# Performance work log

Measured on AMD Instinct MI355X. Metric: run time of the kernel, lower is better.

Reference implementation:

```python
import jax, jax.numpy as jnp
import numpy as np

B, C, H, W = 2, 128, 64, 64
D_STATE = 16
EXPAND = 2
D_INNER = C * EXPAND          # 256
DT_RANK = -(-C // 16)         # 8
K = 4                         # scan directions
COMPRESS = 3
SQUEEZE = 30
EPS = 1e-5


def layernorm(x, g, b):
    mu = x.mean(-1, keepdims=True)
    xm = x - mu
    var = (xm * xm).mean(-1, keepdims=True)
    return xm * jax.lax.rsqrt(var + EPS) * g + b


def conv2d(x, w, bias, pad):
    y = jax.lax.conv_general_dilated(x, w, (1, 1), ((pad, pad), (pad, pad)),
                                     dimension_numbers=('NCHW', 'OIHW', 'NCHW'))
    return y + bias[None, :, None, None]


def selective_scan(xs, dts, A, Bs, Cs):
    # xs,dts: (B,K,D,L); A: (K,D,N); Bs,Cs: (B,K,N,L)
    dt_t = jnp.moveaxis(dts, -1, 0)
    x_t = jnp.moveaxis(xs, -1, 0)
    B_t = jnp.moveaxis(Bs, -1, 0)
    C_t = jnp.moveaxis(Cs, -1, 0)
    h0 = jnp.zeros(xs.shape[:3] + (A.shape[-1],), xs.dtype)

    def step(h, inp):
        dt_l, x_l, b_l, c_l = inp          # (B,K,D),(B,K,D),(B,K,N),(B,K,N)
        dA = jnp.exp(dt_l[..., None] * A)  # (B,K,D,N)
        h = dA * h + (dt_l * x_l)[..., None] * b_l[:, :, None, :]
        y = jnp.einsum('bkdn,bkn->bkd', h, c_l)
        return h, y

    _, ys = jax.lax.scan(step, h0, (dt_t, x_t, B_t, C_t))
    return jnp.moveaxis(ys, 0, -1)  # (B,K,D,L)


def ss2d(x, p):  # x: (B,H,W,C) -> (B,H,W,C)
    xz = x @ p['in_proj_w'].T
    xc, z = jnp.split(xz, 2, axis=-1)
    xc = xc.transpose(0, 3, 1, 2)  # (B,D,H,W)
    xc = jax.lax.conv_general_dilated(xc, p['conv_w'], (1, 1), ((1, 1), (1, 1)),
                                      feature_group_count=D_INNER,
                                      dimension_numbers=('NCHW', 'OIHW', 'NCHW'))
    xc = jax.nn.silu(xc + p['conv_b'][None, :, None, None])
    b, d, h, w = xc.shape
    L = h * w
    x_hw = xc.reshape(b, d, L)
    x_wh = xc.transpose(0, 1, 3, 2).reshape(b, d, L)
    xs = jnp.stack([x_hw, x_wh, x_hw[..., ::-1], x_wh[..., ::-1]], axis=1)  # (B,4,D,L)
    x_dbl = jnp.einsum('bkdl,kcd->bkcl', xs, p['x_proj_w'])
    dtr, Bs, Cs = jnp.split(x_dbl, [DT_RANK, DT_RANK + D_STATE], axis=2)
    dts = jnp.einsum('bkrl,kdr->bkdl', dtr, p['dt_w'])
    dts = jax.nn.softplus(dts + p['dt_b'][None, :, :, None])
    A = -jnp.exp(p['A_logs']).reshape(K, d, D_STATE)
    ys = selective_scan(xs, dts, A, Bs, Cs)
    ys = ys + xs * p['Ds'].reshape(K, d)[None, :, :, None]
    inv = ys[:, 2:4][..., ::-1]  # undo flipped scans
    wh = lambda t: t.reshape(b, d, w, h).transpose(0, 1, 3, 2).reshape(b, d, L)
    y = ys[:, 0] + inv[:, 0] + wh(ys[:, 1]) + wh(inv[:, 1])
    y = y.transpose(0, 2, 1).reshape(b, h, w, d)
    y = layernorm(y, p['out_norm_g'], p['out_norm_b'])
    y = y * jax.nn.silu(z)
    return y @ p['out_proj_w'].T


def cab(x, p):  # x: (B,C,H,W)
    t = jax.nn.gelu(conv2d(x, p['cab_w1'], p['cab_b1'], 1), approximate=False)
    t = conv2d(t, p['cab_w2'], p['cab_b2'], 1)
    s = t.mean((2, 3), keepdims=True)
    s = jax.nn.relu(conv2d(s, p['ca_w1'], p['ca_b1'], 0))
    s = jax.nn.sigmoid(conv2d(s, p['ca_w2'], p['ca_b2'], 0))
    return t * s


def vss_block(input, p):
    inp = input.transpose(0, 2, 3, 1)  # (B,H,W,C)
    x = inp * p['skip_scale'] + ss2d(layernorm(inp, p['ln1_g'], p['ln1_b']), p)
    c = cab(layernorm(x, p['ln2_g'], p['ln2_b']).transpose(0, 3, 1, 2), p)
    x = x * p['skip_scale2'] + c.transpose(0, 2, 3, 1)
    return x.transpose(0, 3, 1, 2)


def setup_inputs() -> dict:
    key = jax.random.key(0)
    ks = jax.random.split(key, 16)
    rn = lambda i, shp, s=0.02: jax.random.normal(ks[i], shp, jnp.float32) * s
    return {
        'input': jax.random.normal(ks[0], (B, C, H, W), jnp.float32),
        'ln1_g': jnp.ones((C,), jnp.float32), 'ln1_b': jnp.zeros((C,), jnp.float32),
        'skip_scale': jnp.ones((C,), jnp.float32), 'skip_scale2': jnp.ones((C,), jnp.float32),
        'ln2_g': jnp.ones((C,), jnp.float32), 'ln2_b': jnp.zeros((C,), jnp.float32),
        'in_proj_w': rn(1, (2 * D_INNER, C)),
        'conv_w': rn(2, (D_INNER, 1, 3, 3), 0.1),
        'conv_b': jnp.zeros((D_INNER,), jnp.float32),
        'x_proj_w': rn(3, (K, DT_RANK + 2 * D_STATE, D_INNER)),
        'dt_w': rn(4, (K, D_INNER, DT_RANK), 0.1),
        'dt_b': rn(5, (K, D_INNER), 0.1),
        'A_logs': jnp.log(jnp.tile(jnp.arange(1, D_STATE + 1, dtype=jnp.float32), (K * D_INNER, 1))),
        'Ds': jnp.ones((K * D_INNER,), jnp.float32),
        'out_norm_g': jnp.ones((D_INNER,), jnp.float32), 'out_norm_b': jnp.zeros((D_INNER,), jnp.float32),
        'out_proj_w': rn(6, (C, D_INNER)),
        'cab_w1': rn(7, (C // COMPRESS, C, 3, 3), 0.05),
        'cab_b1': jnp.zeros((C // COMPRESS,), jnp.float32),
        'cab_w2': rn(8, (C, C // COMPRESS, 3, 3), 0.05),
        'cab_b2': jnp.zeros((C,), jnp.float32),
        'ca_w1': rn(9, (C // SQUEEZE, C, 1, 1), 0.05),
        'ca_b1': jnp.zeros((C // SQUEEZE,), jnp.float32),
        'ca_w2': rn(10, (C, C // SQUEEZE, 1, 1), 0.05),
        'ca_b2': jnp.zeros((C,), jnp.float32),
    }


def reference(input, ln1_g, ln1_b, skip_scale, skip_scale2, ln2_g, ln2_b,
              in_proj_w, conv_w, conv_b, x_proj_w, dt_w, dt_b, A_logs, Ds,
              out_norm_g, out_norm_b, out_proj_w,
              cab_w1, cab_b1, cab_w2, cab_b2, ca_w1, ca_b1, ca_w2, ca_b2):
    p = dict(ln1_g=ln1_g, ln1_b=ln1_b, skip_scale=skip_scale, skip_scale2=skip_scale2,
             ln2_g=ln2_g, ln2_b=ln2_b, in_proj_w=in_proj_w, conv_w=conv_w, conv_b=conv_b,
             x_proj_w=x_proj_w, dt_w=dt_w, dt_b=dt_b, A_logs=A_logs, Ds=Ds,
             out_norm_g=out_norm_g, out_norm_b=out_norm_b, out_proj_w=out_proj_w,
             cab_w1=cab_w1, cab_b1=cab_b1, cab_w2=cab_w2, cab_b2=cab_b2,
             ca_w1=ca_w1, ca_b1=ca_b1, ca_w2=ca_w2, ca_b2=ca_b2)
    return vss_block(input, p)
```

## Files before the change

### kernel.cpp

```cpp
#include <hip/hip_runtime.h>
#include <math.h>

#define BB 2
#define CC 128
#define HH 64
#define WW 64
#define LL 4096
#define DI 256
#define NS 16
#define KK 4
#define OC1 42

#define NC 256
#define CL 16

#define K3_POS 16
#define BCW 48

__device__ __forceinline__ float sigmoidf_(float x) { return 1.f / (1.f + __expf(-x)); }
__device__ __forceinline__ float siluf_(float x)    { return x * sigmoidf_(x); }

__device__ __forceinline__ int scan_pos(int k, int i) {
  if (k == 0) return i;
  if (k == 1) return ((i & 63) << 6) | (i >> 6);
  if (k == 2) return (LL - 1) - i;
  int j = (LL - 1) - i;
  return ((j & 63) << 6) | (j >> 6);
}

__global__ __launch_bounds__(256) void k1_ln_inproj(
    const float* __restrict__ inp, const float* __restrict__ g, const float* __restrict__ b,
    const float* __restrict__ wproj, float* __restrict__ xcin, float* __restrict__ zbuf) {
  __shared__ float sx[64][132];
  __shared__ float sw[128][68];
  __shared__ float smu[64], srs[64];
  const int tid = threadIdx.x;
  const int rt = blockIdx.x & 3;
  const int pt = blockIdx.x >> 2;
  const int bb = pt >> 6;
  const int pbase = (pt & 63) << 6;

  for (int idx = tid; idx < 64 * CC; idx += 256) {
    int c = idx >> 6, pl = idx & 63;
    sx[pl][c] = inp[((size_t)bb * CC + c) * LL + pbase + pl];
  }
  __syncthreads();
  {
    int pl = tid >> 2, j = tid & 3;
    float s = 0.f, s2 = 0.f;
    for (int c = j; c < CC; c += 4) { float v = sx[pl][c]; s += v; s2 += v * v; }
    s += __shfl_xor(s, 1); s2 += __shfl_xor(s2, 1);
    s += __shfl_xor(s, 2); s2 += __shfl_xor(s2, 2);
    if (j == 0) {
      float mu = s * (1.f / CC);
      smu[pl] = mu;
      srs[pl] = rsqrtf(s2 * (1.f / CC) - mu * mu + 1e-5f);
    }
  }
  __syncthreads();
  for (int idx = tid; idx < 64 * CC; idx += 256) {
    int c = idx & 127, pl = idx >> 7;
    sx[pl][c] = (sx[pl][c] - smu[pl]) * srs[pl] * g[c] + b[c];
  }

  const int pg = tid & 7, rg = tid >> 3;
  float acc[8][4];
#pragma unroll
  for (int j = 0; j < 8; j++)
#pragma unroll
    for (int q = 0; q < 4; q++) acc[j][q] = 0.f;

  for (int kc = 0; kc < CC; kc += 64) {
    __syncthreads();
    for (int idx = tid; idx < 128 * 64; idx += 256) {
      int cl = idx & 63, rl = idx >> 6;
      sw[rl][cl] = wproj[(size_t)(rt * 128 + rl) * CC + kc + cl];
    }
    __syncthreads();
#pragma unroll 4
    for (int i = 0; i < 16; i++) {
      const int k0 = kc + 4 * i, kl0 = 4 * i;
      float4 xv[8], wv[4];
#pragma unroll
      for (int j = 0; j < 8; j++) xv[j] = *(const float4*)&sx[pg + 8 * j][k0];
#pragma unroll
      for (int q = 0; q < 4; q++) wv[q] = *(const float4*)&sw[rg + 32 * q][kl0];
#pragma unroll
      for (int j = 0; j < 8; j++)
#pragma unroll
        for (int q = 0; q < 4; q++) {
          acc[j][q] += xv[j].x * wv[q].x + xv[j].y * wv[q].y
                     + xv[j].z * wv[q].z + xv[j].w * wv[q].w;
        }
    }
  }

  float* buf = (rt < 2) ? xcin : zbuf;
  const int drow = (rt & 1) * 128;
#pragma unroll
  for (int j = 0; j < 8; j++) {
    const int p = pbase + pg + 8 * j;
    float* dst = buf + ((size_t)bb * LL + p) * DI + drow;
#pragma unroll
    for (int q = 0; q < 4; q++) dst[rg + 32 * q] = acc[j][q];
  }
}

__global__ __launch_bounds__(256) void k2_dwconv(
    const float* __restrict__ xcin, const float* __restrict__ cw, const float* __restrict__ cb,
    float* __restrict__ xconv) {
  const int w0 = (blockIdx.x & 7) * 8;
  const int hh = (blockIdx.x >> 3) & 63;
  const int bb = blockIdx.x >> 9;
  const int d = threadIdx.x;

  float wv[9];
#pragma unroll
  for (int kk = 0; kk < 9; kk++) wv[kk] = cw[d * 9 + kk];
  const float bias = cb[d];

  float xin[3][10];
#pragma unroll
  for (int kh = 0; kh < 3; kh++) {
    int r = hh + kh - 1;
    bool vr = (r >= 0 && r < HH);
#pragma unroll
    for (int c = 0; c < 10; c++) {
      int cc2 = w0 + c - 1;
      bool vc = (cc2 >= 0 && cc2 < WW);
      xin[kh][c] = (vr && vc) ? xcin[((size_t)bb * LL + r * WW + cc2) * DI + d] : 0.f;
    }
  }
#pragma unroll
  for (int j = 0; j < 8; j++) {
    float acc = bias;
#pragma unroll
    for (int kh = 0; kh < 3; kh++)
#pragma unroll
      for (int kw = 0; kw < 3; kw++)
        acc += wv[kh * 3 + kw] * xin[kh][j + kw];
    xconv[((size_t)bb * LL + hh * WW + w0 + j) * DI + d] = siluf_(acc);
  }
}

__global__ __launch_bounds__(256) void k3_proj(
    const float* __restrict__ xconv, const float* __restrict__ xpw,
    float* __restrict__ BCbuf) {
  __shared__ float sv[K3_POS][260];
  const int tid = threadIdx.x;
  const int bb = blockIdx.x >> 8;
  const int pbase = (blockIdx.x & 255) << 4;

  for (int idx = tid; idx < K3_POS * DI; idx += 256) {
    int d = idx & 255, pl = idx >> 8;
    sv[pl][d] = xconv[((size_t)bb * LL + pbase + pl) * DI + d];
  }
  __syncthreads();

  const int rb = tid >> 4, pg = tid & 15;
  const int r0 = rb * 10;
  float acc[10];
#pragma unroll
  for (int q = 0; q < 10; q++) acc[q] = 0.f;

  const float4* wf = (const float4*)xpw;
#pragma unroll 4
  for (int i = 0; i < DI / 4; i++) {
    float4 xv = *(const float4*)&sv[pg][i * 4];
#pragma unroll
    for (int q = 0; q < 10; q++) {
      float4 wa = wf[(size_t)(r0 + q) * 64 + i];
      acc[q] += wa.x * xv.x + wa.y * xv.y + wa.z * xv.z + wa.w * xv.w;
    }
  }

  const int k = r0 / 40, c0 = r0 - k * 40;
  float* dst = BCbuf + ((size_t)(bb * KK + k) * LL + pbase + pg) * BCW + c0;
#pragma unroll
  for (int q = 0; q < 10; q++) dst[q] = acc[q];
}

__global__ __launch_bounds__(256) void k4a_chunk(
    const float* __restrict__ xconv, const float* __restrict__ BCbuf,
    const float* __restrict__ A_logs, const float* __restrict__ dtw,
    const float* __restrict__ dtb,
    float* __restrict__ csA, float* __restrict__ csB) {
  __shared__ float sBC[CL][26];
  const int d = threadIdx.x;
  const int chunk = blockIdx.x & (NC - 1);
  const int t = blockIdx.x / NC;
  const int k = t & 3;
  const int bb = t >> 2;
  const int bk = bb * KK + k;
  const int base = chunk * CL;

  for (int idx = d; idx < CL * 24; idx += 256) {
    int ii = idx / 24, j = idx - ii * 24;
    int pos = scan_pos(k, base + ii);
    sBC[ii][j] = BCbuf[((size_t)bk * LL + pos) * BCW + j];
  }
  float a[NS];
  bool fast = true;
#pragma unroll
  for (int n = 0; n < NS; n++) {
    a[n] = -__expf(A_logs[((size_t)k * DI + d) * NS + n]);
    fast = fast && (fabsf(a[n] + (float)(n + 1)) < 1e-3f * (n + 1));
  }
  const float* wdt = dtw + ((size_t)k * DI + d) * 8;
  const float4 wd0 = *(const float4*)wdt;
  const float4 wd1 = *(const float4*)(wdt + 4);
  const float bdt = dtb[k * DI + d];
  __syncthreads();

  const float* x_p = xconv + (size_t)bb * LL * DI + d;

  float Ap[NS], Bc[NS];
#pragma unroll
  for (int n = 0; n < NS; n++) { Ap[n] = 1.f; Bc[n] = 0.f; }

  if (fast) {
    float sumdt = 0.f;
#pragma unroll
    for (int half = 0; half < CL / 8; half++) {
      float xvr[8];
#pragma unroll
      for (int j = 0; j < 8; j++)
        xvr[j] = x_p[(size_t)scan_pos(k, base + half * 8 + j) * DI];
#pragma unroll
      for (int j = 0; j < 8; j++) {
        const int ii = half * 8 + j;
        const float* dr = sBC[ii];
        float u = bdt + wd0.x * dr[0] + wd0.y * dr[1] + wd0.z * dr[2] + wd0.w * dr[3]
                      + wd1.x * dr[4] + wd1.y * dr[5] + wd1.z * dr[6] + wd1.w * dr[7];
        float t2 = __expf(u);
        float E = __builtin_amdgcn_rcpf(1.f + t2);
        float dt = u > 20.f ? u : -0.69314718056f * __log2f(E);
        sumdt += dt;
        float dtx = dt * xvr[j];
        float E2 = E * E;
        float dA1 = E, dA2 = E2;
#pragma unroll
        for (int n = 0; n < NS; n += 2) {
          Bc[n] = dA1 * Bc[n] + dtx * sBC[ii][8 + n];
          Bc[n + 1] = dA2 * Bc[n + 1] + dtx * sBC[ii][9 + n];
          dA1 *= E2; dA2 *= E2;
        }
      }
    }
    float Et = __expf(-sumdt);
    float p = Et;
#pragma unroll
    for (int n = 0; n < NS; n++) { Ap[n] = p; p *= Et; }
  } else {
#pragma unroll 2
    for (int ii = 0; ii < CL; ii++) {
      int pos = scan_pos(k, base + ii);
      float xv = x_p[(size_t)pos * DI];
      const float* dr = sBC[ii];
      float u = bdt + wd0.x * dr[0] + wd0.y * dr[1] + wd0.z * dr[2] + wd0.w * dr[3]
                    + wd1.x * dr[4] + wd1.y * dr[5] + wd1.z * dr[6] + wd1.w * dr[7];
      float t2 = __expf(u);
      float dt = u > 20.f ? u : log1pf(t2);
      float dtx = dt * xv;
#pragma unroll
      for (int n = 0; n < NS; n++) {
        float dA = __expf(dt * a[n]);
        Ap[n] *= dA;
        Bc[n] = dA * Bc[n] + dtx * sBC[ii][8 + n];
      }
    }
  }
  size_t e = ((size_t)(bk * NC + chunk) * NS) * DI + d;
#pragma unroll
  for (int n = 0; n < NS; n++) {
    csA[e + (size_t)n * DI] = Ap[n];
    csB[e + (size_t)n * DI] = Bc[n];
  }
}

__global__ __launch_bounds__(256) void k4b_scanchunks(
    float* csAh, const float* __restrict__ csB) {
  const int d = threadIdx.x;
  const int n = blockIdx.x & (NS - 1);
  const int bk = blockIdx.x >> 4;
  const size_t stride = (size_t)NS * DI;
  size_t e = ((size_t)bk * NC * NS + n) * DI + d;
  float H = 0.f;
  for (int c0 = 0; c0 < NC; c0 += 16) {
    float A[16], Bv[16];
#pragma unroll
    for (int j = 0; j < 16; j++) {
      A[j]  = csAh[e + (size_t)j * stride];
      Bv[j] = csB[e + (size_t)j * stride];
    }
#pragma unroll
    for (int j = 0; j < 16; j++) {
      csAh[e + (size_t)j * stride] = H;
      H = A[j] * H + Bv[j];
    }
    e += (size_t)16 * stride;
  }
}

__global__ __launch_bounds__(256) void k4c_scan(
    const float* __restrict__ xconv, const float* __restrict__ BCbuf,
    const float* __restrict__ A_logs, const float* __restrict__ dtw,
    const float* __restrict__ dtb, const float* __restrict__ Ds,
    const float* __restrict__ hin, float* __restrict__ ys) {
  __shared__ float sBC[CL][BCW];
  const int d = threadIdx.x;
  const int chunk = blockIdx.x & (NC - 1);
  const int t = blockIdx.x / NC;
  const int k = t & 3;
  const int bb = t >> 2;
  const int bk = bb * KK + k;
  const int base = chunk * CL;

  for (int idx = d; idx < CL * 40; idx += 256) {
    int ii = idx / 40, j = idx - ii * 40;
    int pos = scan_pos(k, base + ii);
    sBC[ii][j] = BCbuf[((size_t)bk * LL + pos) * BCW + j];
  }
  float a[NS], h[NS];
  bool fast = true;
  const size_t eh = ((size_t)(bk * NC + chunk) * NS) * DI + d;
#pragma unroll
  for (int n = 0; n < NS; n++) {
    a[n] = -__expf(A_logs[((size_t)k * DI + d) * NS + n]);
    fast = fast && (fabsf(a[n] + (float)(n + 1)) < 1e-3f * (n + 1));
    h[n] = hin[eh + (size_t)n * DI];
  }
  const float* wdt = dtw + ((size_t)k * DI + d) * 8;
  const float4 wd0 = *(const float4*)wdt;
  const float4 wd1 = *(const float4*)(wdt + 4);
  const float bdt = dtb[k * DI + d];
  const float Dd = Ds[k * DI + d];
  __syncthreads();

  const float* x_p = xconv + (size_t)bb * LL * DI + d;
  float* ys_p = ys + (size_t)bk * LL * DI + d;

  if (fast) {
#pragma unroll
    for (int half = 0; half < CL / 8; half++) {
      float xvr[8];
#pragma unroll
      for (int j = 0; j < 8; j++)
        xvr[j] = x_p[(size_t)scan_pos(k, base + half * 8 + j) * DI];
#pragma unroll
      for (int j = 0; j < 8; j++) {
        const int ii = half * 8 + j;
        const float* dr = sBC[ii];
        float u = bdt + wd0.x * dr[0] + wd0.y * dr[1] + wd0.z * dr[2] + wd0.w * dr[3]
                      + wd1.x * dr[4] + wd1.y * dr[5] + wd1.z * dr[6] + wd1.w * dr[7];
        float t2 = __expf(u);
        float E = __builtin_amdgcn_rcpf(1.f + t2);
        float dt = u > 20.f ? u : -0.69314718056f * __log2f(E);
        float dtx = dt * xvr[j];
        float y = xvr[j] * Dd;
        float E2 = E * E;
        float dA1 = E, dA2 = E2;
#pragma unroll
        for (int n = 0; n < NS; n += 2) {
          h[n] = dA1 * h[n] + dtx * sBC[ii][8 + n];
          y += h[n] * sBC[ii][24 + n];
          h[n + 1] = dA2 * h[n + 1] + dtx * sBC[ii][9 + n];
          y += h[n + 1] * sBC[ii][25 + n];
          dA1 *= E2; dA2 *= E2;
        }
        ys_p[(size_t)scan_pos(k, base + ii) * DI] = y;
      }
    }
  } else {
#pragma unroll 2
    for (int ii = 0; ii < CL; ii++) {
      int pos = scan_pos(k, base + ii);
      float xv = x_p[(size_t)pos * DI];
      const float* dr = sBC[ii];
      float u = bdt + wd0.x * dr[0] + wd0.y * dr[1] + wd0.z * dr[2] + wd0.w * dr[3]
                    + wd1.x * dr[4] + wd1.y * dr[5] + wd1.z * dr[6] + wd1.w * dr[7];
      float t2 = __expf(u);
      float dt = u > 20.f ? u : log1pf(t2);
      float dtx = dt * xv;
      float y = xv * Dd;
#pragma unroll
      for (int n = 0; n < NS; n++) {
        float dA = __expf(dt * a[n]);
        h[n] = dA * h[n] + dtx * sBC[ii][8 + n];
        y += h[n] * sBC[ii][24 + n];
      }
      ys_p[(size_t)pos * DI] = y;
    }
  }
}

__global__ __launch_bounds__(256) void k5a_act(
    const float* __restrict__ ys, const float* __restrict__ zbuf,
    const float* __restrict__ ong, const float* __restrict__ onb,
    float* __restrict__ yact) {
  __shared__ float sy[8][260];
  __shared__ float smu[8], srs[8];
  const int tid = threadIdx.x;
  const int bb = blockIdx.x >> 9;
  const int pbase = (blockIdx.x & 511) << 3;

  for (int idx = tid; idx < 8 * DI; idx += 256) {
    int d = idx & 255, pl = idx >> 8;
    size_t o0 = (((size_t)bb * KK + 0) * LL + pbase + pl) * DI + d;
    const size_t st = (size_t)LL * DI;
    sy[pl][d] = ys[o0] + ys[o0 + st] + ys[o0 + 2 * st] + ys[o0 + 3 * st];
  }
  __syncthreads();
  {
    int pl = tid >> 5, j = tid & 31;
    float s = 0.f, s2 = 0.f;
    for (int d = j; d < DI; d += 32) { float v = sy[pl][d]; s += v; s2 += v * v; }
#pragma unroll
    for (int m = 1; m < 32; m <<= 1) { s += __shfl_xor(s, m); s2 += __shfl_xor(s2, m); }
    if (j == 0) {
      float mu = s * (1.f / DI);
      smu[pl] = mu;
      srs[pl] = rsqrtf(s2 * (1.f / DI) - mu * mu + 1e-5f);
    }
  }
  __syncthreads();
  for (int idx = tid; idx < 8 * DI; idx += 256) {
    int d = idx & 255, pl = idx >> 8;
    float zv = zbuf[((size_t)bb * LL + pbase + pl) * DI + d];
    yact[((size_t)bb * LL + pbase + pl) * DI + d] =
        ((sy[pl][d] - smu[pl]) * srs[pl] * ong[d] + onb[d]) * siluf_(zv);
  }
}

__global__ __launch_bounds__(256) void k5b_proj(
    const float* __restrict__ yact, const float* __restrict__ opw,
    const float* __restrict__ inp, const float* __restrict__ sk,
    const float* __restrict__ g2, const float* __restrict__ b2,
    float* __restrict__ xres, float* __restrict__ ln2) {
  __shared__ float sx[16][68];
  __shared__ float sw[128][68];
  __shared__ float sr[16][132];
  __shared__ float smu[16], srs[16];
  const int tid = threadIdx.x;
  const int bb = blockIdx.x >> 8;
  const int pbase = (blockIdx.x & 255) << 4;

  const int pg = tid & 7, rb = tid >> 3;
  float acc[2][4];
#pragma unroll
  for (int j = 0; j < 2; j++)
#pragma unroll
    for (int q = 0; q < 4; q++) acc[j][q] = 0.f;

  for (int kc = 0; kc < DI; kc += 64) {
    __syncthreads();
    for (int idx = tid; idx < 16 * 64; idx += 256) {
      int cl = idx & 63, pl = idx >> 6;
      sx[pl][cl] = yact[((size_t)bb * LL + pbase + pl) * DI + kc + cl];
    }
    for (int idx = tid; idx < 128 * 64; idx += 256) {
      int cl = idx & 63, rl = idx >> 6;
      sw[rl][cl] = opw[(size_t)rl * DI + kc + cl];
    }
    __syncthreads();
#pragma unroll 4
    for (int i = 0; i < 16; i++) {
      float4 xv[2], wv[4];
#pragma unroll
      for (int j = 0; j < 2; j++) xv[j] = *(const float4*)&sx[2 * pg + j][4 * i];
#pragma unroll
      for (int q = 0; q < 4; q++) wv[q] = *(const float4*)&sw[rb + 32 * q][4 * i];
#pragma unroll
      for (int j = 0; j < 2; j++)
#pragma unroll
        for (int q = 0; q < 4; q++) {
          acc[j][q] += xv[j].x * wv[q].x + xv[j].y * wv[q].y
                     + xv[j].z * wv[q].z + xv[j].w * wv[q].w;
        }
    }
  }

#pragma unroll
  for (int j = 0; j < 2; j++) {
    const int p = pbase + 2 * pg + j;
#pragma unroll
    for (int q = 0; q < 4; q++) {
      const int c = rb + 32 * q;
      float r = inp[((size_t)bb * CC + c) * LL + p] * sk[c] + acc[j][q];
      xres[((size_t)bb * LL + p) * CC + c] = r;
      sr[2 * pg + j][c] = r;
    }
  }
  __syncthreads();
  {
    int pl = tid >> 4, jj = tid & 15;
    float s = 0.f, s2 = 0.f;
    for (int c = jj; c < CC; c += 16) { float v = sr[pl][c]; s += v; s2 += v * v; }
#pragma unroll
    for (int m = 1; m < 16; m <<= 1) { s += __shfl_xor(s, m); s2 += __shfl_xor(s2, m); }
    if (jj == 0) {
      float mu = s * (1.f / CC);
      smu[pl] = mu;
      srs[pl] = rsqrtf(s2 * (1.f / CC) - mu * mu + 1e-5f);
    }
  }
  __syncthreads();
  for (int idx = tid; idx < 16 * CC; idx += 256) {
    int pl = idx & 15, c = idx >> 4;
    ln2[((size_t)bb * CC + c) * LL + pbase + pl] =
        (sr[pl][c] - smu[pl]) * srs[pl] * g2[c] + b2[c];
  }
}

__global__ __launch_bounds__(256) void k6a_conv1(
    const float* __restrict__ ln2, const float* __restrict__ w1,
    float* __restrict__ pc1) {
  __shared__ float sIn[16][6][68];
  __shared__ float sw[16 * 9 * OC1];
  const int tid = threadIdx.x;
  const int icq = blockIdx.x & 7;
  const int h4  = (blockIdx.x >> 3) & 15;
  const int bb  = blockIdx.x >> 7;
  const int icb = icq * 16;

  for (int idx = tid; idx < 16 * 6 * 66; idx += 256) {
    int i = idx / 396, rem = idx % 396;
    int rr = rem / 66, j = rem % 66;
    int r = h4 * 4 + rr - 1, c2 = j - 1;
    float v = 0.f;
    if (r >= 0 && r < HH && c2 >= 0 && c2 < WW)
      v = ln2[((size_t)bb * CC + icb + i) * LL + r * WW + c2];
    sIn[i][rr][j] = v;
  }
  for (int idx = tid; idx < OC1 * 16 * 9; idx += 256) {
    int oc = idx / 144, rem = idx % 144;
    int i = rem / 9, kk = rem % 9;
    sw[(i * 9 + kk) * OC1 + oc] = w1[((size_t)oc * CC + icb + i) * 9 + kk];
  }
  __syncthreads();

  const int wq = tid & 7, hq = (tid >> 3) & 3, ocg = tid >> 5;
  float acc[6][8];
#pragma unroll
  for (int q = 0; q < 6; q++)
#pragma unroll
    for (int ww = 0; ww < 8; ww++) acc[q][ww] = 0.f;

  for (int i = 0; i < 16; i++) {
    float xin[3][10];
#pragma unroll
    for (int kh = 0; kh < 3; kh++)
#pragma unroll
      for (int j = 0; j < 10; j++) xin[kh][j] = sIn[i][hq + kh][wq * 8 + j];
#pragma unroll
    for (int q = 0; q < 6; q++) {
      int oc = ocg + 8 * q;
      if (oc >= OC1) break;
      float wv[9];
#pragma unroll
      for (int kk = 0; kk < 9; kk++) wv[kk] = sw[(i * 9 + kk) * OC1 + oc];
#pragma unroll
      for (int kh = 0; kh < 3; kh++)
#pragma unroll
        for (int kw = 0; kw < 3; kw++)
#pragma unroll
          for (int ww = 0; ww < 8; ww++)
            acc[q][ww] += wv[kh * 3 + kw] * xin[kh][ww + kw];
    }
  }

  const int hrow = h4 * 4 + hq;
#pragma unroll
  for (int q = 0; q < 6; q++) {
    int oc = ocg + 8 * q;
    if (oc >= OC1) break;
    float* dst = pc1 + (((size_t)icq * BB + bb) * OC1 + oc) * LL + hrow * WW + wq * 8;
    *(float4*)dst       = make_float4(acc[q][0], acc[q][1], acc[q][2], acc[q][3]);
    *(float4*)(dst + 4) = make_float4(acc[q][4], acc[q][5], acc[q][6], acc[q][7]);
  }
}

__global__ __launch_bounds__(256) void k6b_reduce(
    const float* __restrict__ pc1, const float* __restrict__ b1,
    float* __restrict__ t1) {
  const int oc = blockIdx.x % OC1;
  const int bb = blockIdx.x / OC1;
  const float bias = b1[oc];
  const size_t st = (size_t)BB * OC1 * LL;
  const float* src = pc1 + ((size_t)bb * OC1 + oc) * LL;
  float* dst = t1 + ((size_t)bb * OC1 + oc) * LL;
  for (int i = threadIdx.x; i < LL / 4; i += 256) {
    float4 s = ((const float4*)src)[i];
#pragma unroll
    for (int icq = 1; icq < 8; icq++) {
      float4 v = *(const float4*)(src + (size_t)icq * st + i * 4);
      s.x += v.x; s.y += v.y; s.z += v.z; s.w += v.w;
    }
    float r[4] = {s.x + bias, s.y + bias, s.z + bias, s.w + bias};
#pragma unroll
    for (int q = 0; q < 4; q++)
      r[q] = 0.5f * r[q] * (1.f + erff(r[q] * 0.70710678118654752f));
    ((float4*)dst)[i] = make_float4(r[0], r[1], r[2], r[3]);
  }
}

__global__ __launch_bounds__(256) void k7_conv2(
    const float* __restrict__ t1, const float* __restrict__ w2, const float* __restrict__ b2,
    float* __restrict__ t2) {
  __shared__ float sIn[21][4][68];
  __shared__ float sw[21 * 9 * 32];
  const int tid = threadIdx.x;
  const int ocq = blockIdx.x & 3;
  const int h2  = (blockIdx.x >> 2) & 31;
  const int bb  = blockIdx.x >> 7;

  const int wq = tid & 7, hq = (tid >> 3) & 1, ocg = tid >> 4;
  float acc[2][8];
#pragma unroll
  for (int q = 0; q < 2; q++)
#pragma unroll
    for (int ww = 0; ww < 8; ww++) acc[q][ww] = 0.f;

  for (int ch = 0; ch < 2; ch++) {
    const int icb = ch * 21;
    __syncthreads();
    for (int idx = tid; idx < 21 * 4 * 66; idx += 256) {
      int i = idx / 264, rem = idx % 264;
      int rr = rem / 66, j = rem % 66;
      int r = h2 * 2 + rr - 1, c2 = j - 1;
      float v = 0.f;
      if (r >= 0 && r < HH && c2 >= 0 && c2 < WW)
        v = t1[((size_t)bb * OC1 + icb + i) * LL + r * WW + c2];
      sIn[i][rr][j] = v;
    }
    for (int idx = tid; idx < 32 * 21 * 9; idx += 256) {
      int ol = idx / 189, rem = idx % 189;
      int i = rem / 9, kk = rem % 9;
      sw[(i * 9 + kk) * 32 + ol] = w2[((size_t)(ocq * 32 + ol) * OC1 + icb + i) * 9 + kk];
    }
    __syncthreads();

    for (int i = 0; i < 21; i++) {
      float xin[3][10];
#pragma unroll
      for (int kh = 0; kh < 3; kh++)
#pragma unroll
        for (int j = 0; j < 10; j++) xin[kh][j] = sIn[i][hq + kh][wq * 8 + j];
#pragma unroll
      for (int q = 0; q < 2; q++) {
        int ol = ocg + 16 * q;
        float wv[9];
#pragma unroll
        for (int kk = 0; kk < 9; kk++) wv[kk] = sw[(i * 9 + kk) * 32 + ol];
#pragma unroll
        for (int kh = 0; kh < 3; kh++)
#pragma unroll
          for (int kw = 0; kw < 3; kw++)
#pragma unroll
            for (int ww = 0; ww < 8; ww++)
              acc[q][ww] += wv[kh * 3 + kw] * xin[kh][ww + kw];
      }
    }
  }

  const int hrow = h2 * 2 + hq;
#pragma unroll
  for (int q = 0; q < 2; q++) {
    int oc = ocq * 32 + ocg + 16 * q;
    float bias = b2[oc];
    float* dst = t2 + ((size_t)bb * CC + oc) * LL + hrow * WW + wq * 8;
    *(float4*)dst       = make_float4(acc[q][0] + bias, acc[q][1] + bias,
                                      acc[q][2] + bias, acc[q][3] + bias);
    *(float4*)(dst + 4) = make_float4(acc[q][4] + bias, acc[q][5] + bias,
                                      acc[q][6] + bias, acc[q][7] + bias);
  }
}

__global__ __launch_bounds__(256) void k8_mean(const float* __restrict__ t2,
                                               float* __restrict__ smean) {
  __shared__ float red[4];
  const int bc = blockIdx.x;
  const float* src = t2 + (size_t)bc * LL;
  float s = 0.f;
  for (int i = threadIdx.x; i < LL; i += 256) s += src[i];
#pragma unroll
  for (int m = 1; m < 64; m <<= 1) s += __shfl_xor(s, m);
  if ((threadIdx.x & 63) == 0) red[threadIdx.x >> 6] = s;
  __syncthreads();
  if (threadIdx.x == 0) smean[bc] = (red[0] + red[1] + red[2] + red[3]) * (1.f / LL);
}

__global__ __launch_bounds__(256) void k10_final(
    const float* __restrict__ xres, const float* __restrict__ t2,
    const float* __restrict__ smean,
    const float* __restrict__ cw1, const float* __restrict__ cb1,
    const float* __restrict__ cw2, const float* __restrict__ cb2,
    const float* __restrict__ sk2, float* __restrict__ out) {
  __shared__ float mid[4];
  const int tid = threadIdx.x;
  const int bc = blockIdx.x;
  const int bb = bc >> 7, c = bc & 127;

  {
    const int wv = tid >> 6, ln = tid & 63;
    float s = cw1[wv * CC + ln] * smean[bb * CC + ln]
            + cw1[wv * CC + 64 + ln] * smean[bb * CC + 64 + ln];
#pragma unroll
    for (int m = 1; m < 64; m <<= 1) s += __shfl_xor(s, m);
    if (ln == 0) mid[wv] = fmaxf(s + cb1[wv], 0.f);
  }
  __syncthreads();
  float a = cb2[c];
#pragma unroll
  for (int m = 0; m < 4; m++) a += cw2[c * 4 + m] * mid[m];
  const float sv = sigmoidf_(a);

  const float ss = sk2[c];
  const float* t2r = t2 + (size_t)bc * LL;
  float* outr = out + (size_t)bc * LL;
  for (int i = tid; i < LL; i += 256)
    outr[i] = xres[((size_t)bb * LL + i) * CC + c] * ss + t2r[i] * sv;
}


extern "C" void kernel_launch(void* const* d_in, const int* in_sizes, int n_in,
                              void* d_out, int out_size, void* d_ws, size_t ws_size,
                              hipStream_t stream) {
  const float* input      = (const float*)d_in[0];
  const float* ln1_g      = (const float*)d_in[1];
  const float* ln1_b      = (const float*)d_in[2];
  const float* skip_scale = (const float*)d_in[3];
  const float* skip_scale2= (const float*)d_in[4];
  const float* ln2_g      = (const float*)d_in[5];
  const float* ln2_b      = (const float*)d_in[6];
  const float* in_proj_w  = (const float*)d_in[7];
  const float* conv_w     = (const float*)d_in[8];
  const float* conv_b     = (const float*)d_in[9];
  const float* x_proj_w   = (const float*)d_in[10];
  const float* dt_w       = (const float*)d_in[11];
  const float* dt_b       = (const float*)d_in[12];
  const float* A_logs     = (const float*)d_in[13];
  const float* Ds         = (const float*)d_in[14];
  const float* out_norm_g = (const float*)d_in[15];
  const float* out_norm_b = (const float*)d_in[16];
  const float* out_proj_w = (const float*)d_in[17];
  const float* cab_w1     = (const float*)d_in[18];
  const float* cab_b1     = (const float*)d_in[19];
  const float* cab_w2     = (const float*)d_in[20];
  const float* cab_b2     = (const float*)d_in[21];
  const float* ca_w1      = (const float*)d_in[22];
  const float* ca_b1      = (const float*)d_in[23];
  const float* ca_w2      = (const float*)d_in[24];
  const float* ca_b2      = (const float*)d_in[25];

  float* ws = (float*)d_ws;
  float* xcin  = ws;
  float* zbuf  = xcin + (size_t)BB * LL * DI;
  float* xconv = zbuf + (size_t)BB * LL * DI;
  float* BCbuf = xconv + (size_t)BB * LL * DI;
  float* ysb   = BCbuf + (size_t)BB * KK * LL * BCW;
  float* xres  = ysb + (size_t)BB * KK * LL * DI;
  float* ln2b  = xres + (size_t)BB * LL * CC;
  float* t1b   = ln2b + (size_t)BB * CC * LL;
  float* t2b   = t1b + (size_t)BB * OC1 * LL;
  float* smean = t2b + (size_t)BB * CC * LL;
  float* csA   = smean + BB * CC;
  float* csB   = ysb;
  float* pc1   = ysb;
  float* yact  = csA;

  k1_ln_inproj<<<512, 256, 0, stream>>>(input, ln1_g, ln1_b, in_proj_w, xcin, zbuf);
  k2_dwconv<<<BB * HH * (WW / 8), 256, 0, stream>>>(xcin, conv_w, conv_b, xconv);
  k3_proj<<<BB * (LL / K3_POS), 256, 0, stream>>>(xconv, x_proj_w, BCbuf);
  k4a_chunk<<<BB * KK * NC, 256, 0, stream>>>(xconv, BCbuf, A_logs, dt_w, dt_b, csA, csB);
  k4b_scanchunks<<<BB * KK * NS, 256, 0, stream>>>(csA, csB);
  k4c_scan<<<BB * KK * NC, 256, 0, stream>>>(xconv, BCbuf, A_logs, dt_w, dt_b, Ds, csA, ysb);
  k5a_act<<<BB * (LL / 8), 256, 0, stream>>>(ysb, zbuf, out_norm_g, out_norm_b, yact);
  k5b_proj<<<BB * (LL / 16), 256, 0, stream>>>(yact, out_proj_w, input, skip_scale,
                                               ln2_g, ln2_b, xres, ln2b);
  k6a_conv1<<<BB * 16 * 8, 256, 0, stream>>>(ln2b, cab_w1, pc1);
  k6b_reduce<<<BB * OC1, 256, 0, stream>>>(pc1, cab_b1, t1b);
  k7_conv2<<<BB * 32 * 4, 256, 0, stream>>>(t1b, cab_w2, cab_b2, t2b);
  k8_mean<<<BB * CC, 256, 0, stream>>>(t2b, smean);
  k10_final<<<BB * CC, 256, 0, stream>>>(xres, t2b, smean, ca_w1, ca_b1, ca_w2, ca_b2,
                                         skip_scale2, (float*)d_out);
}
```

Before: 274.5 us.

## Tile x_proj kernel over input channels with shared-memory weight staging

```diff
diff --git a/kernel.cpp b/kernel.cpp
--- a/kernel.cpp
+++ b/kernel.cpp
@@ -146,38 +146,57 @@
 __global__ __launch_bounds__(256) void k3_proj(
     const float* __restrict__ xconv, const float* __restrict__ xpw,
     float* __restrict__ BCbuf) {
-  __shared__ float sv[K3_POS][260];
+  __shared__ float sx[16][68];
+  __shared__ float sw[160][68];
   const int tid = threadIdx.x;
   const int bb = blockIdx.x >> 8;
   const int pbase = (blockIdx.x & 255) << 4;
 
-  for (int idx = tid; idx < K3_POS * DI; idx += 256) {
-    int d = idx & 255, pl = idx >> 8;
-    sv[pl][d] = xconv[((size_t)bb * LL + pbase + pl) * DI + d];
-  }
-  __syncthreads();
-
-  const int rb = tid >> 4, pg = tid & 15;
-  const int r0 = rb * 10;
-  float acc[10];
-#pragma unroll
-  for (int q = 0; q < 10; q++) acc[q] = 0.f;
-
-  const float4* wf = (const float4*)xpw;
+  const int pg = tid & 7, rb = tid >> 3;
+  float acc[2][5];
+#pragma unroll
+  for (int j = 0; j < 2; j++)
+#pragma unroll
+    for (int q = 0; q < 5; q++) acc[j][q] = 0.f;
+
+  for (int kc = 0; kc < DI; kc += 64) {
+    __syncthreads();
+    for (int idx = tid; idx < 16 * 64; idx += 256) {
+      int cl = idx & 63, pl = idx >> 6;
+      sx[pl][cl] = xconv[((size_t)bb * LL + pbase + pl) * DI + kc + cl];
+    }
+    for (int idx = tid; idx < 160 * 64; idx += 256) {
+      int cl = idx & 63, rl = idx >> 6;
+      sw[rl][cl] = xpw[(size_t)rl * DI + kc + cl];
+    }
+    __syncthreads();
 #pragma unroll 4
-  for (int i = 0; i < DI / 4; i++) {
-    float4 xv = *(const float4*)&sv[pg][i * 4];
-#pragma unroll
-    for (int q = 0; q < 10; q++) {
-      float4 wa = wf[(size_t)(r0 + q) * 64 + i];
-      acc[q] += wa.x * xv.x + wa.y * xv.y + wa.z * xv.z + wa.w * xv.w;
-    }
-  }
-
-  const int k = r0 / 40, c0 = r0 - k * 40;
-  float* dst = BCbuf + ((size_t)(bb * KK + k) * LL + pbase + pg) * BCW + c0;
-#pragma unroll
-  for (int q = 0; q < 10; q++) dst[q] = acc[q];
+    for (int i = 0; i < 16; i++) {
+      float4 xv[2], wv[5];
+#pragma unroll
+      for (int j = 0; j < 2; j++) xv[j] = *(const float4*)&sx[2 * pg + j][4 * i];
+#pragma unroll
+      for (int q = 0; q < 5; q++) wv[q] = *(const float4*)&sw[rb + 32 * q][4 * i];
+#pragma unroll
+      for (int j = 0; j < 2; j++)
+#pragma unroll
+        for (int q = 0; q < 5; q++) {
+          acc[j][q] += xv[j].x * wv[q].x + xv[j].y * wv[q].y
+                     + xv[j].z * wv[q].z + xv[j].w * wv[q].w;
+        }
+    }
+  }
+
+#pragma unroll
+  for (int j = 0; j < 2; j++) {
+    const int p = pbase + 2 * pg + j;
+#pragma unroll
+    for (int q = 0; q < 5; q++) {
+      const int r = rb + 32 * q;
+      const int k = r / 40, c0 = r - k * 40;
+      BCbuf[((size_t)(bb * KK + k) * LL + p) * BCW + c0] = acc[j][q];
+    }
+  }
 }
 
 __global__ __launch_bounds__(256) void k4a_chunk(
```

New measurement: 263.8 us. -3.9%, faster.
